# Optimization experiments

Hardware: AMD Instinct MI355X
Metric: run time of the kernel (lower is better)

The kernel has to match this reference:

```python
import jax, jax.numpy as jnp
import numpy as np

N_NODES = 100000
N_EDGES = 1600000
N_FEAT = 165
HIDDEN = 128
N_CLASSES = 2
NEG_SLOPE = 0.2


def setup_inputs() -> dict:
    key = jax.random.key(0)
    ks = jax.random.split(key, 16)
    s = 0.05
    return {
        'x': jax.random.normal(ks[0], (N_NODES, N_FEAT), jnp.float32),
        'edge_src': jax.random.randint(ks[1], (N_EDGES,), 0, N_NODES, jnp.int32),
        'edge_dst': jax.random.randint(ks[2], (N_EDGES,), 0, N_NODES, jnp.int32),
        'W1l': jax.random.normal(ks[3], (N_FEAT, HIDDEN), jnp.float32) * s,
        'b1l': jnp.zeros((HIDDEN,), jnp.float32),
        'W1r': jax.random.normal(ks[4], (N_FEAT, HIDDEN), jnp.float32) * s,
        'b1r': jnp.zeros((HIDDEN,), jnp.float32),
        'att1': jax.random.normal(ks[5], (HIDDEN,), jnp.float32) * s,
        'bias1': jnp.zeros((HIDDEN,), jnp.float32),
        'W2l': jax.random.normal(ks[6], (HIDDEN, N_CLASSES), jnp.float32) * s,
        'b2l': jnp.zeros((N_CLASSES,), jnp.float32),
        'W2r': jax.random.normal(ks[7], (HIDDEN, N_CLASSES), jnp.float32) * s,
        'b2r': jnp.zeros((N_CLASSES,), jnp.float32),
        'att2': jax.random.normal(ks[8], (N_CLASSES,), jnp.float32) * s,
        'bias2': jnp.zeros((N_CLASSES,), jnp.float32),
    }


def gatv2_conv(x, src, dst, Wl, bl, Wr, br, att, bias, n_nodes):
    # PyG GATv2Conv, heads=1: x_l for source/message, x_r for target
    xl = x @ Wl + bl            # [N, D_out]
    xr = x @ Wr + br            # [N, D_out]
    e = jax.nn.leaky_relu(xl[src] + xr[dst], NEG_SLOPE)  # [E, D_out]
    score = e @ att             # [E]
    # segment softmax over destination nodes (stable)
    m = jax.ops.segment_max(score, dst, num_segments=n_nodes)
    a = jnp.exp(score - m[dst])
    denom = jax.ops.segment_sum(a, dst, num_segments=n_nodes)
    alpha = a / denom[dst]      # [E]
    out = jax.ops.segment_sum(alpha[:, None] * xl[src], dst, num_segments=n_nodes)
    return out + bias


def reference(x, edge_src, edge_dst, W1l, b1l, W1r, b1r, att1, bias1,
              W2l, b2l, W2r, b2r, att2, bias2):
    n = x.shape[0]
    # GATv2Conv adds self loops by default; every node has >=1 incoming edge
    loops = jnp.arange(n, dtype=edge_src.dtype)
    src = jnp.concatenate([edge_src, loops])
    dst = jnp.concatenate([edge_dst, loops])
    h = gatv2_conv(x, src, dst, W1l, b1l, W1r, b1r, att1, bias1, n)
    h = jax.nn.relu(h)
    # F.dropout with training=False is identity (eval mode)
    out = gatv2_conv(h, src, dst, W2l, b2l, W2r, b2r, att2, bias2, n)
    return out
```

## Files before the change

### kernel.cpp

```cpp
#include <hip/hip_runtime.h>
#include <hip/hip_bf16.h>

#define N_NODES 100000
#define NPAD 100032
#define N_EDGES 1600000
#define ETOT (N_EDGES + N_NODES)
#define NFEAT 165
#define KP 192
#define HID 128
#define NCLS 2
#define NEG 0.2f

#define NBUCK 391
#define CHUNK 16384
#define NCHUNK 104
#define SCAN_PT 20
#define GS_BLOCKS 2048

typedef short bf16x8 __attribute__((ext_vector_type(8)));
typedef float f32x4 __attribute__((ext_vector_type(4)));

#define OFF_FLAG 0
#define OFF_W 16
#define WO_ATT1 42496
#define WO_BIAS1 42624
#define WO_W2L 42752
#define WO_B2L 43008
#define WO_W2R 43010
#define WO_B2R 43266
#define WO_ATT2 43268
#define WO_BIAS2 43270

#define OFF_XB   43392
#define OFF_W2A  OFF_XB
#define OFF_WT   (OFF_XB + NPAD * KP / 2)
#define OFF_BCAT (OFF_WT + 256 * KP / 2)
#define OFF_XLB  (OFF_BCAT + 256)
#define OFF_XRB  (OFF_XLB + NPAD * HID / 2)
#define OFF_PAIRS (OFF_XRB + NPAD * HID / 2)
#define OFF_CSR  (OFF_PAIRS + 2 * ETOT)
#define OFF_ROWPTR (OFF_CSR + ETOT)
#define OFF_S    (OFF_ROWPTR + N_NODES + 8)
#define OFF_XL2  (OFF_S + NBUCK * NCHUNK + 8)
#define OFF_XR2  (OFF_XL2 + N_NODES * NCLS)
#define OFF_H    (OFF_XR2 + N_NODES * NCLS)
#define OFF_DL   (OFF_H + N_NODES * HID)
#define OFF_DR   (OFF_DL + NPAD)

__device__ __forceinline__ float bload16(unsigned short u) {
    return __uint_as_float(((unsigned)u) << 16);
}

__device__ __forceinline__ float lrelu(float v) {
    return fmaf(0.4f, fabsf(v), 0.6f * v);
}

__device__ __forceinline__ void unpack8(uint4 q, float* f) {
    f[0] = __uint_as_float(q.x << 16); f[1] = __uint_as_float(q.x & 0xffff0000u);
    f[2] = __uint_as_float(q.y << 16); f[3] = __uint_as_float(q.y & 0xffff0000u);
    f[4] = __uint_as_float(q.z << 16); f[5] = __uint_as_float(q.z & 0xffff0000u);
    f[6] = __uint_as_float(q.w << 16); f[7] = __uint_as_float(q.w & 0xffff0000u);
}

__device__ __forceinline__ unsigned short f2b(float f) {
    __hip_bfloat16 b = __float2bfloat16(f);
    return *(unsigned short*)&b;
}

__device__ __forceinline__ unsigned pack2(float a, float b) {
    return (unsigned)f2b(a) | ((unsigned)f2b(b) << 16);
}

__device__ __forceinline__ unsigned detect_flag(const unsigned short* x16, int lane) {
    unsigned short hh = x16[lane];
    unsigned e = (hh >> 7) & 0xFF;
    bool pl = ((hh & 0x7FFF) == 0) || (e >= 100 && e <= 140);
    unsigned long long m = __ballot(pl);
    return (__popcll(m) >= 52) ? 1u : 0u;
}

#define PREP_WT 49152
#define PREP_BC (PREP_WT + 256)
#define PREP_TOT (PREP_BC + 776)
#define PREP_BLKS ((PREP_TOT + 255) / 256)
__global__ void __launch_bounds__(256) k_prep_hist(
        const int* __restrict__ edst, int* __restrict__ bh,
        const unsigned short* __restrict__ x16,
        const void* W1l, const void* b1l, const void* W1r, const void* b1r,
        const void* att1, const void* bias1, const void* W2l, const void* b2l,
        const void* W2r, const void* b2r, const void* att2, const void* bias2,
        unsigned* __restrict__ flagp, unsigned short* __restrict__ wt,
        float* __restrict__ bcat, float* __restrict__ wb,
        float* __restrict__ w2a) {
    __shared__ int hist[NBUCK];
    if (blockIdx.x < NCHUNK) {
        for (int i = threadIdx.x; i < NBUCK; i += 256) hist[i] = 0;
        __syncthreads();
        int base = blockIdx.x * CHUNK;
        for (int i = threadIdx.x; i < CHUNK; i += 256) {
            int e = base + i;
            if (e >= ETOT) break;
            int d = (e < N_EDGES) ? edst[e] : (e - N_EDGES);
            atomicAdd(&hist[d >> 8], 1);
        }
        __syncthreads();
        for (int b = threadIdx.x; b < NBUCK; b += 256)
            bh[b * NCHUNK + blockIdx.x] = hist[b];
        return;
    }
    int lane = threadIdx.x & 63;
    unsigned isbf = detect_flag(x16, lane);
    int i = (blockIdx.x - NCHUNK) * 256 + threadIdx.x;
    if (i == 0) *flagp = isbf;
    if (i >= PREP_TOT) return;
    if (i < PREP_WT) {
        int n = i / KP, k = i - n * KP;
        unsigned short v = 0;
        if (k < NFEAT) {
            const void* src = (n < HID) ? W1l : W1r;
            size_t off = (size_t)k * HID + (n & (HID - 1));
            v = isbf ? ((const unsigned short*)src)[off]
                     : f2b(((const float*)src)[off]);
        }
        wt[i] = v;
    } else if (i < PREP_BC) {
        int n = i - PREP_WT;
        const void* src = (n < HID) ? b1l : b1r;
        int off = n & (HID - 1);
        bcat[n] = isbf ? bload16(((const unsigned short*)src)[off])
                       : ((const float*)src)[off];
    } else {
        int j = i - PREP_BC;
        const void* src; int off; int dst;
        if      (j < 128) { src = att1;  off = j;       dst = WO_ATT1 + j; }
        else if (j < 256) { src = bias1; off = j - 128; dst = WO_BIAS1 + (j - 128); }
        else if (j < 512) { src = W2l;   off = j - 256; dst = WO_W2L + (j - 256); }
        else if (j < 514) { src = b2l;   off = j - 512; dst = WO_B2L + (j - 512); }
        else if (j < 770) { src = W2r;   off = j - 514; dst = WO_W2R + (j - 514); }
        else if (j < 772) { src = b2r;   off = j - 770; dst = WO_B2R + (j - 770); }
        else if (j < 774) { src = att2;  off = j - 772; dst = WO_ATT2 + (j - 772); }
        else              { src = bias2; off = j - 774; dst = WO_BIAS2 + (j - 774); }
        float val = isbf ? bload16(((const unsigned short*)src)[off])
                         : ((const float*)src)[off];
        wb[dst] = val;
        if (j >= 256 && j < 512) w2a[j - 256] = val;
        else if (j >= 514 && j < 770) w2a[256 + (j - 514)] = val;
    }
}

__global__ void __launch_bounds__(512) k_pa_scan(int* __restrict__ S,
                                                 int* __restrict__ rowptr) {
    __shared__ int lds[512];
    const int TOT4 = (NBUCK * NCHUNK) / 4;
    int t = threadIdx.x;
    int b4 = t * SCAN_PT;
    uint4* S4 = (uint4*)S;
    int sum = 0;
    for (int k = 0; k < SCAN_PT; k++) {
        int i = b4 + k;
        if (i < TOT4) {
            uint4 v = S4[i];
            sum += (int)(v.x + v.y + v.z + v.w);
        }
    }
    lds[t] = sum;
    __syncthreads();
    for (int off = 1; off < 512; off <<= 1) {
        int v = lds[t];
        if (t >= off) v += lds[t - off];
        __syncthreads();
        lds[t] = v;
        __syncthreads();
    }
    int carry = (t == 0) ? 0 : lds[t - 1];
    for (int k = 0; k < SCAN_PT; k++) {
        int i = b4 + k;
        if (i < TOT4) {
            uint4 v = S4[i];
            uint4 o;
            o.x = carry; carry += v.x;
            o.y = carry; carry += v.y;
            o.z = carry; carry += v.z;
            o.w = carry; carry += v.w;
            S4[i] = o;
        }
    }
    if (t == 0) rowptr[N_NODES] = ETOT;
}

__global__ void __launch_bounds__(256) k_scatter(const int* __restrict__ esrc,
                                                 const int* __restrict__ edst,
                                                 const int* __restrict__ S,
                                                 unsigned* __restrict__ pairs) {
    __shared__ int cur[NBUCK];
    for (int i = threadIdx.x; i < NBUCK; i += 256)
        cur[i] = S[i * NCHUNK + blockIdx.x];
    __syncthreads();
    int base = blockIdx.x * CHUNK;
    for (int i = threadIdx.x; i < CHUNK; i += 256) {
        int e = base + i;
        if (e >= ETOT) break;
        int s = (e < N_EDGES) ? esrc[e] : (e - N_EDGES);
        int d = (e < N_EDGES) ? edst[e] : (e - N_EDGES);
        int p = atomicAdd(&cur[d >> 8], 1);
        pairs[p] = (unsigned)s | ((unsigned)(d & 255) << 24);
    }
}

#define XS_STRIDE 200
__global__ void __launch_bounds__(256) k_gemm1(
        const void* __restrict__ x, const unsigned* __restrict__ flagp,
        const unsigned short* __restrict__ wt, const float* __restrict__ bcat,
        const float* __restrict__ attp,
        __hip_bfloat16* __restrict__ xlb, __hip_bfloat16* __restrict__ xrb,
        float* __restrict__ dl, float* __restrict__ dr) {
    __shared__ struct { unsigned short xs[64 * XS_STRIDE]; float dpart[4][64]; } u;
    int tid = threadIdx.x;
    int wave = tid >> 6, lane = tid & 63;
    int quad = lane >> 4, li = lane & 15;
    int node0 = blockIdx.x * 64;
    unsigned isbf = *flagp;
    const float* xf = (const float*)x;
    const unsigned short* x16 = (const unsigned short*)x;

    for (int i = tid; i < 64 * 27; i += 256) {
        int r = i / 27, c = 165 + (i - r * 27);
        u.xs[r * XS_STRIDE + c] = 0;
    }
    if (node0 + 64 <= N_NODES) {
        if (isbf) {
            const uint4* src = (const uint4*)(x16 + (size_t)node0 * NFEAT);
            for (int i = tid; i < 1320; i += 256) {
                uint4 v = src[i];
                int f = i * 8;
                unsigned short hh[8] = {
                    (unsigned short)(v.x & 0xffff), (unsigned short)(v.x >> 16),
                    (unsigned short)(v.y & 0xffff), (unsigned short)(v.y >> 16),
                    (unsigned short)(v.z & 0xffff), (unsigned short)(v.z >> 16),
                    (unsigned short)(v.w & 0xffff), (unsigned short)(v.w >> 16)};
#pragma unroll
                for (int t = 0; t < 8; t++) {
                    int ff = f + t, r = ff / NFEAT, c = ff - r * NFEAT;
                    u.xs[r * XS_STRIDE + c] = hh[t];
                }
            }
        } else {
            const float4* src = (const float4*)(xf + (size_t)node0 * NFEAT);
            for (int i = tid; i < 2640; i += 256) {
                float4 v = src[i];
                int f = i * 4;
                unsigned short hh[4] = {f2b(v.x), f2b(v.y), f2b(v.z), f2b(v.w)};
#pragma unroll
                for (int t = 0; t < 4; t++) {
                    int ff = f + t, r = ff / NFEAT, c = ff - r * NFEAT;
                    u.xs[r * XS_STRIDE + c] = hh[t];
                }
            }
        }
    } else {
        for (int i = tid; i < 64 * NFEAT; i += 256) {
            int r = i / NFEAT, c = i - r * NFEAT;
            int grow = node0 + r;
            unsigned short v = 0;
            if (grow < N_NODES) {
                size_t g = (size_t)grow * NFEAT + c;
                v = isbf ? x16[g] : f2b(xf[g]);
            }
            u.xs[r * XS_STRIDE + c] = v;
        }
    }

    bf16x8 wfrag[4][6];
#pragma unroll
    for (int q = 0; q < 4; q++) {
        int n = wave * 64 + q * 16 + li;
#pragma unroll
        for (int kk = 0; kk < 6; kk++)
            wfrag[q][kk] = *(const bf16x8*)&wt[(size_t)n * KP + kk * 32 + quad * 8];
    }
    float4 bv[4], attq4[4];
    int colbase = (wave & 1) * 64;
#pragma unroll
    for (int q = 0; q < 4; q++) {
        bv[q] = *(const float4*)&bcat[wave * 64 + q * 16 + quad * 4];
        attq4[q] = *(const float4*)&attp[colbase + q * 16 + quad * 4];
    }
    __syncthreads();

    for (int mt = 0; mt < 4; mt++) {
        bf16x8 xfrag[6];
#pragma unroll
        for (int kk = 0; kk < 6; kk++)
            xfrag[kk] = *(const bf16x8*)&u.xs[(mt * 16 + li) * XS_STRIDE + kk * 32 + quad * 8];
        int node = node0 + mt * 16 + li;
        __hip_bfloat16* dst = (wave < 2) ? xlb : xrb;
        float dp = 0.f;
#pragma unroll
        for (int q = 0; q < 4; q++) {
            f32x4 a = {0.f, 0.f, 0.f, 0.f};
#pragma unroll
            for (int kk = 0; kk < 6; kk++)
                a = __builtin_amdgcn_mfma_f32_16x16x32_bf16(wfrag[q][kk], xfrag[kk], a, 0, 0, 0);
            float f0 = a[0] + bv[q].x, f1 = a[1] + bv[q].y;
            float f2 = a[2] + bv[q].z, f3 = a[3] + bv[q].w;
            dp = fmaf(f0, attq4[q].x, dp);
            dp = fmaf(f1, attq4[q].y, dp);
            dp = fmaf(f2, attq4[q].z, dp);
            dp = fmaf(f3, attq4[q].w, dp);
            uint2 val = { pack2(f0, f1), pack2(f2, f3) };
            int col = colbase + q * 16 + quad * 4;
            *(uint2*)&dst[(size_t)node * HID + col] = val;
        }
        dp += __shfl_xor(dp, 16);
        dp += __shfl_xor(dp, 32);
        if (lane < 16) u.dpart[wave][mt * 16 + li] = dp;
    }
    __syncthreads();
    if (tid < 64)
        dl[node0 + tid] = u.dpart[0][tid] + u.dpart[1][tid];
    else if (tid < 128)
        dr[node0 + tid - 64] = u.dpart[2][tid - 64] + u.dpart[3][tid - 64];
}

__global__ void __launch_bounds__(256) k_bsort(const int* __restrict__ S,
                                               const unsigned* __restrict__ pairs,
                                               int* __restrict__ rowptr,
                                               int* __restrict__ csr) {
    __shared__ int hist[256];
    __shared__ int cur[256];
    int b = blockIdx.x, t = threadIdx.x;
    int beg = S[b * NCHUNK];
    int end = (b == NBUCK - 1) ? ETOT : S[(b + 1) * NCHUNK];
    hist[t] = 0;
    __syncthreads();
    for (int j = beg + t; j < end; j += 256)
        atomicAdd(&hist[pairs[j] >> 24], 1);
    __syncthreads();
    for (int off = 1; off < 256; off <<= 1) {
        int v = hist[t];
        if (t >= off) v += hist[t - off];
        __syncthreads();
        hist[t] = v;
        __syncthreads();
    }
    int excl = (t == 0) ? 0 : hist[t - 1];
    int node = b * 256 + t;
    if (node < N_NODES) rowptr[node] = beg + excl;
    cur[t] = beg + excl;
    __syncthreads();
    for (int j = beg + t; j < end; j += 256) {
        unsigned pr = pairs[j];
        int p = atomicAdd(&cur[pr >> 24], 1);
        csr[p] = (int)(pr & 0xFFFFFFu);
    }
}

__global__ void __launch_bounds__(256) k_gat1(const int* __restrict__ rowptr,
                                              const int* __restrict__ csr,
                                              const __hip_bfloat16* __restrict__ xlb,
                                              const __hip_bfloat16* __restrict__ xrb,
                                              const float* __restrict__ att,
                                              const float* __restrict__ bias,
                                              const float* __restrict__ dotsl,
                                              const float* __restrict__ dotsr,
                                              unsigned short* __restrict__ h16) {
    int wave = threadIdx.x >> 6, lane = threadIdx.x & 63;
    int sub = lane >> 4, li = lane & 15;
    float atv[8];
    {
        float4 t0 = ((const float4*)att)[li * 2];
        float4 t1 = ((const float4*)att)[li * 2 + 1];
        atv[0] = 0.4f * t0.x; atv[1] = 0.4f * t0.y;
        atv[2] = 0.4f * t0.z; atv[3] = 0.4f * t0.w;
        atv[4] = 0.4f * t1.x; atv[5] = 0.4f * t1.y;
        atv[6] = 0.4f * t1.z; atv[7] = 0.4f * t1.w;
    }

    for (int d = blockIdx.x * 4 + wave; d < N_NODES; d += GS_BLOCKS * 4) {
        uint4 qr = ((const uint4*)(xrb + (size_t)d * HID))[li];
        float xrv[8]; unpack8(qr, xrv);
        float drd = dotsr[d];
        int beg = rowptr[d], end = rowptr[d + 1];
        int iters = (end - beg + 3) >> 2;
        float l = 0.f, o[8];
#pragma unroll
        for (int t = 0; t < 8; t++) o[t] = 0.f;

        int j = beg + sub;
        bool valid = j < end;
        int s = valid ? csr[j] : 0;
        uint4 q = *(const uint4*)(xlb + (size_t)s * HID + li * 8);
        float dlc = dotsl[s];

        for (int it = 0; it < iters; it++) {
            float c[8]; unpack8(q, c);
            bool v = valid;
            float dle = dlc;
            j += 4;
            valid = j < end;
            int sn = valid ? csr[j] : 0;
            q = *(const uint4*)(xlb + (size_t)sn * HID + li * 8);
            dlc = dotsl[sn];

            float pa = 0.f;
#pragma unroll
            for (int t = 0; t < 8; t++) {
                float vv = c[t] + xrv[t];
                pa = fmaf(atv[t], fabsf(vv), pa);
            }
            pa += __shfl_xor(pa, 1);
            pa += __shfl_xor(pa, 2);
            pa += __shfl_xor(pa, 4);
            pa += __shfl_xor(pa, 8);
            float p = fmaf(0.6f, dle + drd, pa);
            float a = v ? __expf(p) : 0.f;
            l += a;
#pragma unroll
            for (int t = 0; t < 8; t++) o[t] = fmaf(a, c[t], o[t]);
        }
        l += __shfl_xor(l, 16);
        l += __shfl_xor(l, 32);
#pragma unroll
        for (int t = 0; t < 8; t++) {
            o[t] += __shfl_xor(o[t], 16);
            o[t] += __shfl_xor(o[t], 32);
        }
        if (sub == 0) {
            float inv = 1.f / l;
            float4 bv0 = ((const float4*)bias)[li * 2];
            float4 bv1 = ((const float4*)bias)[li * 2 + 1];
            float r0 = fmaxf(fmaf(o[0], inv, bv0.x), 0.f);
            float r1 = fmaxf(fmaf(o[1], inv, bv0.y), 0.f);
            float r2 = fmaxf(fmaf(o[2], inv, bv0.z), 0.f);
            float r3 = fmaxf(fmaf(o[3], inv, bv0.w), 0.f);
            float r4 = fmaxf(fmaf(o[4], inv, bv1.x), 0.f);
            float r5 = fmaxf(fmaf(o[5], inv, bv1.y), 0.f);
            float r6 = fmaxf(fmaf(o[6], inv, bv1.z), 0.f);
            float r7 = fmaxf(fmaf(o[7], inv, bv1.w), 0.f);
            uint4 val = { pack2(r0, r1), pack2(r2, r3),
                          pack2(r4, r5), pack2(r6, r7) };
            *(uint4*)&h16[(size_t)d * HID + li * 8] = val;
        }
    }
}

__global__ void __launch_bounds__(256) k_gemm2(const unsigned short* __restrict__ h16,
                                               const float* __restrict__ wb,
                                               const float* __restrict__ w2a,
                                               float* __restrict__ xl2, float* __restrict__ xr2) {
    int wave = threadIdx.x >> 6, lane = threadIdx.x & 63;
    int node = blockIdx.x * 4 + wave;
    if (node >= N_NODES) return;
    unsigned hw = ((const unsigned*)(h16 + (size_t)node * HID))[lane];
    float h0 = __uint_as_float(hw << 16);
    float h1 = __uint_as_float(hw & 0xffff0000u);
    float4 wl = ((const float4*)w2a)[lane];
    float4 wr = ((const float4*)(w2a + 256))[lane];
    float al0 = h0 * wl.x + h1 * wl.z;
    float al1 = h0 * wl.y + h1 * wl.w;
    float ar0 = h0 * wr.x + h1 * wr.z;
    float ar1 = h0 * wr.y + h1 * wr.w;
#pragma unroll
    for (int off = 32; off > 0; off >>= 1) {
        al0 += __shfl_down(al0, off);
        al1 += __shfl_down(al1, off);
        ar0 += __shfl_down(ar0, off);
        ar1 += __shfl_down(ar1, off);
    }
    if (lane == 0) {
        xl2[node * 2 + 0] = al0 + wb[WO_B2L + 0];
        xl2[node * 2 + 1] = al1 + wb[WO_B2L + 1];
        xr2[node * 2 + 0] = ar0 + wb[WO_B2R + 0];
        xr2[node * 2 + 1] = ar1 + wb[WO_B2R + 1];
    }
}

__global__ void __launch_bounds__(256) k_gat2(const int* __restrict__ rowptr,
                                              const int* __restrict__ csr,
                                              const float* __restrict__ xl2,
                                              const float* __restrict__ xr2,
                                              const float* __restrict__ wb,
                                              const unsigned* __restrict__ flag,
                                              void* __restrict__ dout) {
    int t = blockIdx.x * 256 + threadIdx.x;
    int d = t >> 2, part = t & 3;
    if (d >= N_NODES) return;
    float xr0 = xr2[d * 2 + 0], xr1 = xr2[d * 2 + 1];
    float at0 = wb[WO_ATT2], at1 = wb[WO_ATT2 + 1];
    int beg = rowptr[d], end = rowptr[d + 1];
    float l = 0.f, o0 = 0.f, o1 = 0.f;
    for (int j = beg + part; j < end; j += 4) {
        int s = csr[j];
        float b0 = xl2[s * 2 + 0], b1 = xl2[s * 2 + 1];
        float p = at0 * lrelu(b0 + xr0) + at1 * lrelu(b1 + xr1);
        float a = __expf(p);
        l += a;
        o0 = fmaf(a, b0, o0);
        o1 = fmaf(a, b1, o1);
    }
    l += __shfl_xor(l, 1);  o0 += __shfl_xor(o0, 1);  o1 += __shfl_xor(o1, 1);
    l += __shfl_xor(l, 2);  o0 += __shfl_xor(o0, 2);  o1 += __shfl_xor(o1, 2);
    if (part == 0) {
        float inv = 1.f / l;
        float v0 = fmaf(o0, inv, wb[WO_BIAS2 + 0]);
        float v1 = fmaf(o1, inv, wb[WO_BIAS2 + 1]);
        if (*flag) {
            ((__hip_bfloat16*)dout)[d * 2 + 0] = __float2bfloat16(v0);
            ((__hip_bfloat16*)dout)[d * 2 + 1] = __float2bfloat16(v1);
        } else {
            ((float*)dout)[d * 2 + 0] = v0;
            ((float*)dout)[d * 2 + 1] = v1;
        }
    }
}

extern "C" void kernel_launch(void* const* d_in, const int* in_sizes, int n_in,
                              void* d_out, int out_size, void* d_ws, size_t ws_size,
                              hipStream_t stream) {
    char* w = (char*)d_ws;
    unsigned* flag = (unsigned*)(w + (size_t)OFF_FLAG * 4);
    float* wb = (float*)(w + (size_t)OFF_W * 4);
    float* w2a = (float*)(w + (size_t)OFF_W2A * 4);
    unsigned short* wt = (unsigned short*)(w + (size_t)OFF_WT * 4);
    float* bcat = (float*)(w + (size_t)OFF_BCAT * 4);
    __hip_bfloat16* xlb = (__hip_bfloat16*)(w + (size_t)OFF_XLB * 4);
    __hip_bfloat16* xrb = (__hip_bfloat16*)(w + (size_t)OFF_XRB * 4);
    unsigned* pairs = (unsigned*)(w + (size_t)OFF_PAIRS * 4);
    int* csr = (int*)(w + (size_t)OFF_CSR * 4);
    int* rowptr = (int*)(w + (size_t)OFF_ROWPTR * 4);
    int* S = (int*)(w + (size_t)OFF_S * 4);
    float* xl2 = (float*)(w + (size_t)OFF_XL2 * 4);
    float* xr2 = (float*)(w + (size_t)OFF_XR2 * 4);
    unsigned short* h16 = (unsigned short*)(w + (size_t)OFF_H * 4);
    float* dl = (float*)(w + (size_t)OFF_DL * 4);
    float* dr = (float*)(w + (size_t)OFF_DR * 4);
    const int* esrc = (const int*)d_in[1];
    const int* edst = (const int*)d_in[2];

    k_prep_hist<<<NCHUNK + PREP_BLKS, 256, 0, stream>>>(
        edst, S, (const unsigned short*)d_in[0],
        d_in[3], d_in[4], d_in[5], d_in[6], d_in[7], d_in[8],
        d_in[9], d_in[10], d_in[11], d_in[12], d_in[13], d_in[14],
        flag, wt, bcat, wb, w2a);

    k_pa_scan<<<1, 512, 0, stream>>>(S, rowptr);

    k_scatter<<<NCHUNK, 256, 0, stream>>>(esrc, edst, S, pairs);

    k_bsort<<<NBUCK, 256, 0, stream>>>(S, pairs, rowptr, csr);

    k_gemm1<<<NPAD / 64, 256, 0, stream>>>(d_in[0], flag, wt, bcat,
                                           wb + WO_ATT1, xlb, xrb, dl, dr);

    k_gat1<<<GS_BLOCKS, 256, 0, stream>>>(rowptr, csr, xlb, xrb,
                                          wb + WO_ATT1, wb + WO_BIAS1,
                                          dl, dr, h16);

    k_gemm2<<<(N_NODES + 3) / 4, 256, 0, stream>>>(h16, wb, w2a, xl2, xr2);

    k_gat2<<<(4 * N_NODES + 255) / 256, 256, 0, stream>>>(rowptr, csr, xl2, xr2,
                                                          wb, flag, d_out);
}
```

Measured before the change: 394.0 us.

## Parallelize bucket-offset scan, shrink edge chunks, pre-pack x into padded bf16

Cuts the edge chunk size by four so the histogram and scatter kernels launch four times as many blocks. The single-block prefix scan becomes a three-kernel multi-block scan (block sums, scan of the sums, final scan). Converting and padding x to bf16 moves out of the GEMM into extra blocks of the prep kernel, so the GEMM reads a padded matrix straight into registers without staging through LDS. This adds two launches and an extra global round-trip of the packed x, in exchange for more parallelism in the sort and a lighter GEMM.

```diff
diff --git a/kernel.cpp b/kernel.cpp
--- a/kernel.cpp
+++ b/kernel.cpp
@@ -12,10 +12,12 @@
 #define NEG 0.2f
 
 #define NBUCK 391
-#define CHUNK 16384
-#define NCHUNK 104
-#define SCAN_PT 20
+#define CHUNK 4096
+#define NCHUNK 416
+#define TOT4 ((NBUCK * NCHUNK) / 4)
+#define NSB ((TOT4 + 511) / 512)
 #define GS_BLOCKS 2048
+#define REPACK_BLKS (NPAD / 64)
 
 typedef short bf16x8 __attribute__((ext_vector_type(8)));
 typedef float f32x4 __attribute__((ext_vector_type(4)));
@@ -32,7 +34,7 @@
 #define WO_BIAS2 43270
 
 #define OFF_XB   43392
-#define OFF_W2A  OFF_XB
+#define OFF_XP   OFF_XB
 #define OFF_WT   (OFF_XB + NPAD * KP / 2)
 #define OFF_BCAT (OFF_WT + 256 * KP / 2)
 #define OFF_XLB  (OFF_BCAT + 256)
@@ -46,6 +48,8 @@
 #define OFF_H    (OFF_XR2 + N_NODES * NCLS)
 #define OFF_DL   (OFF_H + N_NODES * HID)
 #define OFF_DR   (OFF_DL + NPAD)
+#define OFF_W2A  (OFF_DR + NPAD)
+#define OFF_BSUM (OFF_W2A + 512)
 
 __device__ __forceinline__ float bload16(unsigned short u) {
     return __uint_as_float(((unsigned)u) << 16);
@@ -91,7 +95,7 @@
         const void* W2r, const void* b2r, const void* att2, const void* bias2,
         unsigned* __restrict__ flagp, unsigned short* __restrict__ wt,
         float* __restrict__ bcat, float* __restrict__ wb,
-        float* __restrict__ w2a) {
+        float* __restrict__ w2a, unsigned short* __restrict__ xp) {
     __shared__ int hist[NBUCK];
     if (blockIdx.x < NCHUNK) {
         for (int i = threadIdx.x; i < NBUCK; i += 256) hist[i] = 0;
@@ -110,6 +114,35 @@
     }
     int lane = threadIdx.x & 63;
     unsigned isbf = detect_flag(x16, lane);
+    const float* xf = (const float*)x16;
+
+    if (blockIdx.x >= NCHUNK + PREP_BLKS) {
+        int node0 = (blockIdx.x - NCHUNK - PREP_BLKS) * 64;
+        for (int i = threadIdx.x; i < 64 * (KP / 8); i += 256) {
+            int r = i / (KP / 8);
+            int c0 = (i - r * (KP / 8)) * 8;
+            int grow = node0 + r;
+            unsigned short hh[8];
+#pragma unroll
+            for (int j = 0; j < 8; j++) {
+                int c = c0 + j;
+                unsigned short v = 0;
+                if (grow < N_NODES && c < NFEAT) {
+                    size_t g = (size_t)grow * NFEAT + c;
+                    v = isbf ? x16[g] : f2b(xf[g]);
+                }
+                hh[j] = v;
+            }
+            uint4 o;
+            o.x = (unsigned)hh[0] | ((unsigned)hh[1] << 16);
+            o.y = (unsigned)hh[2] | ((unsigned)hh[3] << 16);
+            o.z = (unsigned)hh[4] | ((unsigned)hh[5] << 16);
+            o.w = (unsigned)hh[6] | ((unsigned)hh[7] << 16);
+            *(uint4*)&xp[(size_t)grow * KP + c0] = o;
+        }
+        return;
+    }
+
     int i = (blockIdx.x - NCHUNK) * 256 + threadIdx.x;
     if (i == 0) *flagp = isbf;
     if (i >= PREP_TOT) return;
@@ -148,44 +181,71 @@
     }
 }
 
-__global__ void __launch_bounds__(512) k_pa_scan(int* __restrict__ S,
-                                                 int* __restrict__ rowptr) {
+__global__ void __launch_bounds__(512) k_scan1(const int* __restrict__ S,
+                                               int* __restrict__ bsum) {
     __shared__ int lds[512];
-    const int TOT4 = (NBUCK * NCHUNK) / 4;
     int t = threadIdx.x;
-    int b4 = t * SCAN_PT;
+    int i = blockIdx.x * 512 + t;
+    const uint4* S4 = (const uint4*)S;
+    int v = 0;
+    if (i < TOT4) {
+        uint4 q = S4[i];
+        v = (int)(q.x + q.y + q.z + q.w);
+    }
+    lds[t] = v;
+    __syncthreads();
+    for (int off = 256; off > 0; off >>= 1) {
+        if (t < off) lds[t] += lds[t + off];
+        __syncthreads();
+    }
+    if (t == 0) bsum[blockIdx.x] = lds[0];
+}
+
+__global__ void __launch_bounds__(128) k_scan2(int* __restrict__ bsum) {
+    __shared__ int lds[128];
+    int t = threadIdx.x;
+    int v = (t < NSB) ? bsum[t] : 0;
+    lds[t] = v;
+    __syncthreads();
+    for (int off = 1; off < 128; off <<= 1) {
+        int x = lds[t];
+        if (t >= off) x += lds[t - off];
+        __syncthreads();
+        lds[t] = x;
+        __syncthreads();
+    }
+    if (t < NSB) bsum[t] = (t == 0) ? 0 : lds[t - 1];
+}
+
+__global__ void __launch_bounds__(512) k_scan3(int* __restrict__ S,
+                                               const int* __restrict__ bsum,
+                                               int* __restrict__ rowptr) {
+    __shared__ int lds[512];
+    int t = threadIdx.x, b = blockIdx.x;
+    int i = b * 512 + t;
     uint4* S4 = (uint4*)S;
-    int sum = 0;
-    for (int k = 0; k < SCAN_PT; k++) {
-        int i = b4 + k;
-        if (i < TOT4) {
-            uint4 v = S4[i];
-            sum += (int)(v.x + v.y + v.z + v.w);
-        }
-    }
-    lds[t] = sum;
+    uint4 q = {0, 0, 0, 0};
+    if (i < TOT4) q = S4[i];
+    int s = (int)(q.x + q.y + q.z + q.w);
+    lds[t] = s;
     __syncthreads();
     for (int off = 1; off < 512; off <<= 1) {
-        int v = lds[t];
-        if (t >= off) v += lds[t - off];
-        __syncthreads();
-        lds[t] = v;
-        __syncthreads();
-    }
-    int carry = (t == 0) ? 0 : lds[t - 1];
-    for (int k = 0; k < SCAN_PT; k++) {
-        int i = b4 + k;
-        if (i < TOT4) {
-            uint4 v = S4[i];
-            uint4 o;
-            o.x = carry; carry += v.x;
-            o.y = carry; carry += v.y;
-            o.z = carry; carry += v.z;
-            o.w = carry; carry += v.w;
-            S4[i] = o;
-        }
-    }
-    if (t == 0) rowptr[N_NODES] = ETOT;
+        int x = lds[t];
+        if (t >= off) x += lds[t - off];
+        __syncthreads();
+        lds[t] = x;
+        __syncthreads();
+    }
+    int excl = ((t == 0) ? 0 : lds[t - 1]) + bsum[b];
+    if (i < TOT4) {
+        uint4 o;
+        o.x = excl;
+        o.y = excl + q.x;
+        o.z = excl + q.x + q.y;
+        o.w = excl + q.x + q.y + q.z;
+        S4[i] = o;
+    }
+    if (b == 0 && t == 0) rowptr[N_NODES] = ETOT;
 }
 
 __global__ void __launch_bounds__(256) k_scatter(const int* __restrict__ esrc,
@@ -207,68 +267,17 @@
     }
 }
 
-#define XS_STRIDE 200
 __global__ void __launch_bounds__(256) k_gemm1(
-        const void* __restrict__ x, const unsigned* __restrict__ flagp,
+        const unsigned short* __restrict__ xp,
         const unsigned short* __restrict__ wt, const float* __restrict__ bcat,
         const float* __restrict__ attp,
         __hip_bfloat16* __restrict__ xlb, __hip_bfloat16* __restrict__ xrb,
         float* __restrict__ dl, float* __restrict__ dr) {
-    __shared__ struct { unsigned short xs[64 * XS_STRIDE]; float dpart[4][64]; } u;
+    __shared__ float dpart[4][64];
     int tid = threadIdx.x;
     int wave = tid >> 6, lane = tid & 63;
     int quad = lane >> 4, li = lane & 15;
     int node0 = blockIdx.x * 64;
-    unsigned isbf = *flagp;
-    const float* xf = (const float*)x;
-    const unsigned short* x16 = (const unsigned short*)x;
-
-    for (int i = tid; i < 64 * 27; i += 256) {
-        int r = i / 27, c = 165 + (i - r * 27);
-        u.xs[r * XS_STRIDE + c] = 0;
-    }
-    if (node0 + 64 <= N_NODES) {
-        if (isbf) {
-            const uint4* src = (const uint4*)(x16 + (size_t)node0 * NFEAT);
-            for (int i = tid; i < 1320; i += 256) {
-                uint4 v = src[i];
-                int f = i * 8;
-                unsigned short hh[8] = {
-                    (unsigned short)(v.x & 0xffff), (unsigned short)(v.x >> 16),
-                    (unsigned short)(v.y & 0xffff), (unsigned short)(v.y >> 16),
-                    (unsigned short)(v.z & 0xffff), (unsigned short)(v.z >> 16),
-                    (unsigned short)(v.w & 0xffff), (unsigned short)(v.w >> 16)};
-#pragma unroll
-                for (int t = 0; t < 8; t++) {
-                    int ff = f + t, r = ff / NFEAT, c = ff - r * NFEAT;
-                    u.xs[r * XS_STRIDE + c] = hh[t];
-                }
-            }
-        } else {
-            const float4* src = (const float4*)(xf + (size_t)node0 * NFEAT);
-            for (int i = tid; i < 2640; i += 256) {
-                float4 v = src[i];
-                int f = i * 4;
-                unsigned short hh[4] = {f2b(v.x), f2b(v.y), f2b(v.z), f2b(v.w)};
-#pragma unroll
-                for (int t = 0; t < 4; t++) {
-                    int ff = f + t, r = ff / NFEAT, c = ff - r * NFEAT;
-                    u.xs[r * XS_STRIDE + c] = hh[t];
-                }
-            }
-        }
-    } else {
-        for (int i = tid; i < 64 * NFEAT; i += 256) {
-            int r = i / NFEAT, c = i - r * NFEAT;
-            int grow = node0 + r;
-            unsigned short v = 0;
-            if (grow < N_NODES) {
-                size_t g = (size_t)grow * NFEAT + c;
-                v = isbf ? x16[g] : f2b(xf[g]);
-            }
-            u.xs[r * XS_STRIDE + c] = v;
-        }
-    }
 
     bf16x8 wfrag[4][6];
 #pragma unroll
@@ -285,14 +294,13 @@
         bv[q] = *(const float4*)&bcat[wave * 64 + q * 16 + quad * 4];
         attq4[q] = *(const float4*)&attp[colbase + q * 16 + quad * 4];
     }
-    __syncthreads();
 
     for (int mt = 0; mt < 4; mt++) {
+        int node = node0 + mt * 16 + li;
         bf16x8 xfrag[6];
 #pragma unroll
         for (int kk = 0; kk < 6; kk++)
-            xfrag[kk] = *(const bf16x8*)&u.xs[(mt * 16 + li) * XS_STRIDE + kk * 32 + quad * 8];
-        int node = node0 + mt * 16 + li;
+            xfrag[kk] = *(const bf16x8*)&xp[(size_t)node * KP + kk * 32 + quad * 8];
         __hip_bfloat16* dst = (wave < 2) ? xlb : xrb;
         float dp = 0.f;
 #pragma unroll
@@ -313,13 +321,13 @@
         }
         dp += __shfl_xor(dp, 16);
         dp += __shfl_xor(dp, 32);
-        if (lane < 16) u.dpart[wave][mt * 16 + li] = dp;
+        if (lane < 16) dpart[wave][mt * 16 + li] = dp;
     }
     __syncthreads();
     if (tid < 64)
-        dl[node0 + tid] = u.dpart[0][tid] + u.dpart[1][tid];
+        dl[node0 + tid] = dpart[0][tid] + dpart[1][tid];
     else if (tid < 128)
-        dr[node0 + tid - 64] = u.dpart[2][tid - 64] + u.dpart[3][tid - 64];
+        dr[node0 + tid - 64] = dpart[2][tid - 64] + dpart[3][tid - 64];
 }
 
 __global__ void __launch_bounds__(256) k_bsort(const int* __restrict__ S,
@@ -520,7 +528,7 @@
     char* w = (char*)d_ws;
     unsigned* flag = (unsigned*)(w + (size_t)OFF_FLAG * 4);
     float* wb = (float*)(w + (size_t)OFF_W * 4);
-    float* w2a = (float*)(w + (size_t)OFF_W2A * 4);
+    unsigned short* xp = (unsigned short*)(w + (size_t)OFF_XP * 4);
     unsigned short* wt = (unsigned short*)(w + (size_t)OFF_WT * 4);
     float* bcat = (float*)(w + (size_t)OFF_BCAT * 4);
     __hip_bfloat16* xlb = (__hip_bfloat16*)(w + (size_t)OFF_XLB * 4);
@@ -534,22 +542,26 @@
     unsigned short* h16 = (unsigned short*)(w + (size_t)OFF_H * 4);
     float* dl = (float*)(w + (size_t)OFF_DL * 4);
     float* dr = (float*)(w + (size_t)OFF_DR * 4);
+    float* w2a = (float*)(w + (size_t)OFF_W2A * 4);
+    int* bsum = (int*)(w + (size_t)OFF_BSUM * 4);
     const int* esrc = (const int*)d_in[1];
     const int* edst = (const int*)d_in[2];
 
-    k_prep_hist<<<NCHUNK + PREP_BLKS, 256, 0, stream>>>(
+    k_prep_hist<<<NCHUNK + PREP_BLKS + REPACK_BLKS, 256, 0, stream>>>(
         edst, S, (const unsigned short*)d_in[0],
         d_in[3], d_in[4], d_in[5], d_in[6], d_in[7], d_in[8],
         d_in[9], d_in[10], d_in[11], d_in[12], d_in[13], d_in[14],
-        flag, wt, bcat, wb, w2a);
-
-    k_pa_scan<<<1, 512, 0, stream>>>(S, rowptr);
+        flag, wt, bcat, wb, w2a, xp);
+
+    k_scan1<<<NSB, 512, 0, stream>>>(S, bsum);
+    k_scan2<<<1, 128, 0, stream>>>(bsum);
+    k_scan3<<<NSB, 512, 0, stream>>>(S, bsum, rowptr);
 
     k_scatter<<<NCHUNK, 256, 0, stream>>>(esrc, edst, S, pairs);
 
     k_bsort<<<NBUCK, 256, 0, stream>>>(S, pairs, rowptr, csr);
 
-    k_gemm1<<<NPAD / 64, 256, 0, stream>>>(d_in[0], flag, wt, bcat,
+    k_gemm1<<<NPAD / 64, 256, 0, stream>>>(xp, wt, bcat,
                                            wb + WO_ATT1, xlb, xrb, dl, dr);
 
     k_gat1<<<GS_BLOCKS, 256, 0, stream>>>(rowptr, csr, xlb, xrb,
```

Measured after the change: 368.9 us. 6.4% less time.
